# Optimization experiments

Measured on AMD Instinct MI355X. Metric: run time of the kernel, lower is better.

The kernel has to match this reference:

```python
import jax, jax.numpy as jnp
import numpy as np

B, N, DIN, A = 64, 64, 64, 32
DOUT = 128          # obs_output_dim == obs_act_output_dim == 128 (required by module wiring)
OA_IN = DIN + A     # obs_act_input_dim = 96


def _w(key, shape):
    fan_in = shape[-1]
    return jax.random.normal(key, shape, jnp.float32) / jnp.sqrt(jnp.float32(fan_in))


def setup_inputs() -> dict:
    key = jax.random.key(0)
    ks = jax.random.split(key, 14)
    return {
        "states": jax.random.normal(ks[0], (B, N, DIN), jnp.float32),
        "policies": jax.random.uniform(ks[1], (B, N, A), jnp.float32),
        "actions": jax.random.uniform(ks[2], (B, N, A), jnp.float32),
        # state_embed_preproc: Linear(obs_input_dim, 128) + LeakyReLU
        "W_se_pre": _w(ks[3], (128, DIN)),
        "b_se_pre": jnp.zeros((128,), jnp.float32),
        # key/query layers (shared between both attention stages in forward)
        "W_key": _w(ks[4], (DOUT, 128)),
        "W_query": _w(ks[5], (DOUT, 128)),
        # state_embed: Linear(obs_output_dim, 128) + LeakyReLU
        "W_se": _w(ks[6], (128, DOUT)),
        "b_se": jnp.zeros((128,), jnp.float32),
        # state_act_pol_embed: Linear(obs_act_input_dim, 128) + LeakyReLU
        "W_sap": _w(ks[7], (128, OA_IN)),
        "b_sap": jnp.zeros((128,), jnp.float32),
        # attention_value_layer: Linear(128, obs_act_output_dim)
        "W_av": _w(ks[8], (DOUT, 128)),
        # final value head
        "W_f1": _w(ks[9], (64, DOUT)),
        "W_f2": _w(ks[10], (1, 64)),
    }


def reference(states, policies, actions, W_se_pre, b_se_pre, W_key, W_query,
              W_se, b_se, W_sap, b_sap, W_av, W_f1, W_f2):
    lrelu = jax.nn.leaky_relu  # negative_slope=0.01, matches torch default
    d_k = W_key.shape[0]
    inv_sqrt_dk = 1.0 / jnp.sqrt(jnp.asarray(d_k, states.dtype))

    # stage 1: self-attention over agents on raw-state embeddings
    e = lrelu(states @ W_se_pre.T + b_se_pre)                       # [B,N,128]
    q1 = e @ W_query.T
    k1 = e @ W_key.T
    w_pre = jax.nn.softmax(jnp.einsum('bid,bjd->bij', q1, k1) * inv_sqrt_dk, axis=-1)
    # NB: attention_value_layer_preproc output is overwritten in the original forward;
    # the effective value is weight_preproc @ states_embed_preproc.
    av_pre = jnp.einsum('bij,bjd->bid', w_pre, e)                   # [B,N,128]

    # stage 2: self-attention weights over agents on re-embedded states
    se = lrelu(av_pre @ W_se.T + b_se)                              # [B,N,128]
    q2 = se @ W_query.T
    k2 = se @ W_key.T
    w = jax.nn.softmax(jnp.einsum('bid,bjd->bij', q2, k2) * inv_sqrt_dk, axis=-1)

    # obs_actions_policies[b,j,k] = (state_k, policy_k) if j==k else (state_k, action_k)
    obs_act = jnp.concatenate([states, actions], axis=-1)           # [B,N,OA_IN]
    obs_pol = jnp.concatenate([states, policies], axis=-1)
    n = states.shape[1]
    eye = jnp.eye(n, dtype=states.dtype)[None, :, :, None]          # [1,N,N,1]
    oap = eye * obs_pol[:, None, :, :] + (1.0 - eye) * obs_act[:, None, :, :]  # [B,N,N,OA_IN]

    emb = lrelu(oap @ W_sap.T + b_sap)                              # [B,N,N,128]
    av = emb @ W_av.T                                               # [B,N,N,DOUT]

    # fused form of repeat->weight->sum: node[b,i,j,d] = sum_k w[b,i,k] * av[b,j,k,d]
    node = jnp.einsum('bik,bjkd->bijd', w, av)                      # [B,N,N,DOUT]

    value = lrelu(node @ W_f1.T) @ W_f2.T                           # [B,N,N,1]
    return value, w_pre, w
```

## Files before the change

kernel.cpp:

```cpp
#include <hip/hip_runtime.h>

#define DEVFN __device__ __forceinline__

constexpr int BNN = 64 * 64 * 64;
constexpr float SCALE = 0.08838834764831845f;
constexpr float NSLOPE = 0.01f;

constexpr int OFF_WPRET = 0;
constexpr int OFF_WQT   = 8192;
constexpr int OFF_M     = 24576;
constexpr int OFF_WSET  = 40960;
constexpr int OFF_WSAPT = 57344;
constexpr int OFF_WAVT  = 69632;
constexpr int OFF_WF1T  = 86016;
constexpr int OFF_E     = 98304;
constexpr int OFF_Q     = 622592;
constexpr int OFF_ET    = 1146880;
constexpr int OFF_SET   = 1671168;
constexpr int OFF_HA    = 2195456;
constexpr int OFF_HD    = 2719744;


DEVFN void st128(int tid, const float* __restrict__ src, float* __restrict__ Bs, int rows) {
  const int n4 = rows * 32;
  for (int idx = tid; idx < n4; idx += 512) {
    const int r = idx >> 5, c = idx & 31;
    *reinterpret_cast<float4*>(&Bs[r * 132 + c * 4]) =
        *reinterpret_cast<const float4*>(&src[r * 128 + c * 4]);
  }
}

DEVFN void st64x(int tid, const float* __restrict__ src, float* __restrict__ Bs) {
  for (int idx = tid; idx < 1024; idx += 512) {
    const int r = idx >> 4, c = idx & 15;
    *reinterpret_cast<float4*>(&Bs[r * 68 + c * 4]) =
        *reinterpret_cast<const float4*>(&src[r * 64 + c * 4]);
  }
}

DEVFN void wrT(int tid, const float* __restrict__ S, float* __restrict__ dst, int rq) {
  const int fr = tid >> 2, a4 = tid & 3;
  float t[4];
#pragma unroll
  for (int i = 0; i < 4; ++i) t[i] = S[(a4 * 4 + i) * 132 + fr];
  float4 v; v.x = t[0]; v.y = t[1]; v.z = t[2]; v.w = t[3];
  *reinterpret_cast<float4*>(&dst[fr * 64 + rq * 16 + a4 * 4]) = v;
}


DEVFN void g1(int tid, const float* __restrict__ A, int lda,
              const float* __restrict__ Bs, int K, float (&acc)[4]) {
  const int c0 = (tid & 31) * 4, rg = tid >> 5;
#pragma unroll 8
  for (int k = 0; k < K; ++k) {
    const float4 bv = *reinterpret_cast<const float4*>(&Bs[k * 132 + c0]);
    const float a = A[rg * lda + k];
    acc[0] += a * bv.x; acc[1] += a * bv.y; acc[2] += a * bv.z; acc[3] += a * bv.w;
  }
}

DEVFN void g2A(int tid, const float* __restrict__ A0, const float* __restrict__ A1,
               int lda, const float* __restrict__ Bs, int K,
               float (&a0)[4], float (&a1)[4]) {
  const int c0 = (tid & 31) * 4, rg = tid >> 5;
#pragma unroll 4
  for (int k = 0; k < K; ++k) {
    const float4 bv = *reinterpret_cast<const float4*>(&Bs[k * 132 + c0]);
    const float x = A0[rg * lda + k];
    const float y = A1[rg * lda + k];
    a0[0] += x * bv.x; a0[1] += x * bv.y; a0[2] += x * bv.z; a0[3] += x * bv.w;
    a1[0] += y * bv.x; a1[1] += y * bv.y; a1[2] += y * bv.z; a1[3] += y * bv.w;
  }
}

DEVFN void gH(int tid, const float* __restrict__ A, int lda,
              const float* __restrict__ Bs, int K, float (&acc)[2]) {
  const int c0 = (tid & 31) * 2, rg = tid >> 5;
#pragma unroll 8
  for (int k = 0; k < K; ++k) {
    const float2 bv = *reinterpret_cast<const float2*>(&Bs[k * 68 + c0]);
    const float a = A[rg * lda + k];
    acc[0] += a * bv.x; acc[1] += a * bv.y;
  }
}

DEVFN void gH2(int tid, const float* __restrict__ A0, const float* __restrict__ A1,
               int lda, const float* __restrict__ Bs, int K,
               float (&a0)[2], float (&a1)[2]) {
  const int c0 = (tid & 31) * 2, rg = tid >> 5;
#pragma unroll 4
  for (int k = 0; k < K; ++k) {
    const float2 bv = *reinterpret_cast<const float2*>(&Bs[k * 68 + c0]);
    const float x = A0[rg * lda + k];
    const float y = A1[rg * lda + k];
    a0[0] += x * bv.x; a0[1] += x * bv.y;
    a1[0] += y * bv.x; a1[1] += y * bv.y;
  }
}

template<bool ACT, bool HASB>
DEVFN void epi(int tid, const float (&acc)[4], float* __restrict__ O, int ldo,
               const float* __restrict__ bias) {
  const int c0 = (tid & 31) * 4, rg = tid >> 5;
  float t[4];
#pragma unroll
  for (int i = 0; i < 4; ++i) {
    float x = acc[i];
    if constexpr (HASB) x += bias[c0 + i];
    if constexpr (ACT) x = (x > 0.f) ? x : NSLOPE * x;
    t[i] = x;
  }
  float4 v; v.x = t[0]; v.y = t[1]; v.z = t[2]; v.w = t[3];
  *reinterpret_cast<float4*>(&O[rg * ldo + c0]) = v;
}


DEVFN void score_half(int tid, const float* __restrict__ Qs, int hoff,
                      const float* __restrict__ Ks, float (&acc)[2]) {
  const int j = tid & 63, iw = tid >> 6;
#pragma unroll 2
  for (int kt = 0; kt < 64; kt += 8) {
    float qv[2][8];
#pragma unroll
    for (int r = 0; r < 2; ++r) {
      *reinterpret_cast<float4*>(&qv[r][0]) =
          *reinterpret_cast<const float4*>(&Qs[(iw * 2 + r) * 132 + hoff + kt]);
      *reinterpret_cast<float4*>(&qv[r][4]) =
          *reinterpret_cast<const float4*>(&Qs[(iw * 2 + r) * 132 + hoff + kt + 4]);
    }
#pragma unroll
    for (int kk = 0; kk < 8; ++kk) {
      const float kv = Ks[(kt + kk) * 68 + j];
      acc[0] += qv[0][kk] * kv;
      acc[1] += qv[1][kk] * kv;
    }
  }
}

DEVFN void softmax_write(int tid, float (&acc)[2], float* __restrict__ Wp,
                         float* __restrict__ gout) {
  const int j = tid & 63, iw = tid >> 6;
#pragma unroll
  for (int r = 0; r < 2; ++r) {
    float v = acc[r] * SCALE;
    float m = v;
#pragma unroll
    for (int off = 32; off > 0; off >>= 1) m = fmaxf(m, __shfl_xor(m, off, 64));
    const float p = __expf(v - m);
    float s = p;
#pragma unroll
    for (int off = 32; off > 0; off >>= 1) s += __shfl_xor(s, off, 64);
    const float w = p / s;
    Wp[(iw * 2 + r) * 68 + j] = w;
    gout[(iw * 2 + r) * 64 + j] = w;
  }
}


__global__ void transpose_all(const float* __restrict__ Wpre, const float* __restrict__ Wq,
                              const float* __restrict__ Wse, const float* __restrict__ Wsap,
                              const float* __restrict__ Wav, const float* __restrict__ Wf1,
                              float* __restrict__ ws) {
  const int m = blockIdx.y;
  const float* src; int Cout, K, off;
  switch (m) {
    case 0: src = Wpre; Cout = 128; K = 64;  off = OFF_WPRET; break;
    case 1: src = Wq;   Cout = 128; K = 128; off = OFF_WQT;   break;
    case 2: src = Wse;  Cout = 128; K = 128; off = OFF_WSET;  break;
    case 3: src = Wsap; Cout = 128; K = 96;  off = OFF_WSAPT; break;
    case 4: src = Wav;  Cout = 128; K = 128; off = OFF_WAVT;  break;
    default: src = Wf1; Cout = 64;  K = 128; off = OFF_WF1T;  break;
  }
  const int idx = blockIdx.x * 256 + threadIdx.x;
  if (idx < Cout * K) {
    const int c = idx / K, k = idx - c * K;
    ws[off + k * Cout + c] = src[idx];
  }
}

__global__ __launch_bounds__(512) void make_M(const float* __restrict__ Wkey,
                                              float* __restrict__ ws) {
  __shared__ float As[16 * 132];
  __shared__ float Bs[64 * 132];
  const int tid = threadIdx.x;
  const int r0 = blockIdx.x * 16;
  {
    const int r = tid >> 5, c = tid & 31;
    *reinterpret_cast<float4*>(&As[r * 132 + c * 4]) =
        *reinterpret_cast<const float4*>(&ws[OFF_WQT + (r0 + r) * 128 + c * 4]);
  }
  const int c0 = (tid & 31) * 4, rg = tid >> 5;
  float acc[4] = {};
  for (int h = 0; h < 2; ++h) {
    __syncthreads();
    st128(tid, Wkey + h * 8192, Bs, 64);
    __syncthreads();
#pragma unroll 8
    for (int k = 0; k < 64; ++k) {
      const float4 bv = *reinterpret_cast<const float4*>(&Bs[k * 132 + c0]);
      const float a = As[rg * 132 + h * 64 + k];
      acc[0] += a * bv.x; acc[1] += a * bv.y; acc[2] += a * bv.z; acc[3] += a * bv.w;
    }
  }
  float4 v; v.x = acc[0]; v.y = acc[1]; v.z = acc[2]; v.w = acc[3];
  *reinterpret_cast<float4*>(&ws[OFF_M + (r0 + rg) * 128 + c0]) = v;
}

__global__ __launch_bounds__(512) void P1(const float* __restrict__ states,
                                          const float* __restrict__ policies,
                                          const float* __restrict__ actions,
                                          const float* __restrict__ b_sap,
                                          const float* __restrict__ b_se_pre,
                                          float* __restrict__ ws) {
  __shared__ float S[16 * 68];
  __shared__ float Aa[16 * 36], Ap[16 * 36];
  __shared__ float Ea[16 * 132];
  __shared__ float Ep[16 * 132], Dd[16 * 132], Er[16 * 132];
  __shared__ float Bs[64 * 132];
  const int tid = threadIdx.x;
  const int wid = ((blockIdx.x & 7) << 5) | (blockIdx.x >> 3);
  const int b = wid >> 2, rq = wid & 3;
  const int r0g = b * 64 + rq * 16;

  for (int idx = tid; idx < 1024; idx += 512) {
    const int r = idx >> 6, c = idx & 63;
    S[r * 68 + c] = states[(r0g + r) * 64 + c];
  }
  {
    const int r = tid >> 5, c = tid & 31;
    Aa[r * 36 + c] = actions[(r0g + r) * 32 + c];
    Ap[r * 36 + c] = policies[(r0g + r) * 32 + c];
  }
  st128(tid, ws + OFF_WSAPT, Bs, 64);
  __syncthreads();
  float cm[4] = {};
  g1(tid, S, 68, Bs, 64, cm);
  __syncthreads();
  st128(tid, ws + OFF_WSAPT + 8192, Bs, 32);
  __syncthreads();
  float aa[4] = {cm[0], cm[1], cm[2], cm[3]};
  float ap[4] = {cm[0], cm[1], cm[2], cm[3]};
  g2A(tid, Aa, Ap, 36, Bs, 32, aa, ap);
  epi<true, true>(tid, aa, Ea, 132, b_sap);
  epi<true, true>(tid, ap, Ep, 132, b_sap);
  __syncthreads();
  for (int idx = tid; idx < 2048; idx += 512) {
    const int r = idx >> 7, c = idx & 127;
    Ep[r * 132 + c] -= Ea[r * 132 + c];
  }
  __syncthreads();
  st128(tid, ws + OFF_WAVT, Bs, 64);
  __syncthreads();
  float av[4] = {}, dl[4] = {};
  g2A(tid, Ea, Ep, 132, Bs, 64, av, dl);
  __syncthreads();
  st128(tid, ws + OFF_WAVT + 8192, Bs, 64);
  __syncthreads();
  g2A(tid, Ea + 64, Ep + 64, 132, Bs, 64, av, dl);
  __syncthreads();
  epi<false, false>(tid, av, Ea, 132, nullptr);
  epi<false, false>(tid, dl, Dd, 132, nullptr);
  __syncthreads();
  st64x(tid, ws + OFF_WF1T, Bs);
  __syncthreads();
  float ah[2] = {}, aha[2] = {};
  gH2(tid, Dd, Ea, 132, Bs, 64, ah, aha);
  __syncthreads();
  st64x(tid, ws + OFF_WF1T + 4096, Bs);
  __syncthreads();
  gH2(tid, Dd + 64, Ea + 64, 132, Bs, 64, ah, aha);
  {
    const int c0 = (tid & 31) * 2, rg = tid >> 5;
    float2 vh; vh.x = ah[0]; vh.y = ah[1];
    float2 va; va.x = aha[0]; va.y = aha[1];
    *reinterpret_cast<float2*>(&ws[OFF_HD + (r0g + rg) * 64 + c0]) = vh;
    *reinterpret_cast<float2*>(&ws[OFF_HA + (r0g + rg) * 64 + c0]) = va;
  }
  __syncthreads();
  st128(tid, ws + OFF_WPRET, Bs, 64);
  __syncthreads();
  {
    float ae[4] = {};
    g1(tid, S, 68, Bs, 64, ae);
    const int c0 = (tid & 31) * 4, rg = tid >> 5;
    float t[4];
#pragma unroll
    for (int i = 0; i < 4; ++i) {
      float x = ae[i] + b_se_pre[c0 + i];
      t[i] = (x > 0.f) ? x : NSLOPE * x;
    }
    float4 v; v.x = t[0]; v.y = t[1]; v.z = t[2]; v.w = t[3];
    *reinterpret_cast<float4*>(&Er[rg * 132 + c0]) = v;
    *reinterpret_cast<float4*>(&ws[OFF_E + (r0g + rg) * 128 + c0]) = v;
  }
  __syncthreads();
  wrT(tid, Er, ws + OFF_ET + b * 8192, rq);
  st128(tid, ws + OFF_M, Bs, 64);
  __syncthreads();
  float af[4] = {};
  g1(tid, Er, 132, Bs, 64, af);
  __syncthreads();
  st128(tid, ws + OFF_M + 8192, Bs, 64);
  __syncthreads();
  g1(tid, Er + 64, 132, Bs, 64, af);
  epi<false, false>(tid, af, ws + OFF_Q + r0g * 128, 128, nullptr);
}

__global__ __launch_bounds__(512) void P3(const float* __restrict__ b_se,
                                          float* __restrict__ ws,
                                          float* __restrict__ out) {
  __shared__ float Qs[16 * 132];
  __shared__ float Bs[64 * 132];
  __shared__ float Wp[16 * 68], AV[16 * 132], SEr[16 * 132];
  const int tid = threadIdx.x;
  const int wid = ((blockIdx.x & 7) << 5) | (blockIdx.x >> 3);
  const int b = wid >> 2, rq = wid & 3;
  const int r0g = b * 64 + rq * 16;

  {
    const int r = tid >> 5, c = tid & 31;
    *reinterpret_cast<float4*>(&Qs[r * 132 + c * 4]) =
        *reinterpret_cast<const float4*>(&ws[OFF_Q + (r0g + r) * 128 + c * 4]);
  }
  st64x(tid, ws + OFF_ET + b * 8192, Bs);
  __syncthreads();
  float sc[2] = {};
  score_half(tid, Qs, 0, Bs, sc);
  __syncthreads();
  st64x(tid, ws + OFF_ET + b * 8192 + 4096, Bs);
  __syncthreads();
  score_half(tid, Qs, 64, Bs, sc);
  softmax_write(tid, sc, Wp, out + BNN + b * 4096 + rq * 1024);
  __syncthreads();
  st128(tid, ws + OFF_E + b * 8192, Bs, 64);
  __syncthreads();
  {
    float a[4] = {};
    g1(tid, Wp, 68, Bs, 64, a);
    epi<false, false>(tid, a, AV, 132, nullptr);
  }
  __syncthreads();
  st128(tid, ws + OFF_WSET, Bs, 64);
  __syncthreads();
  float as[4] = {};
  g1(tid, AV, 132, Bs, 64, as);
  __syncthreads();
  st128(tid, ws + OFF_WSET + 8192, Bs, 64);
  __syncthreads();
  g1(tid, AV + 64, 132, Bs, 64, as);
  {
    const int c0 = (tid & 31) * 4, rg = tid >> 5;
    float t[4];
#pragma unroll
    for (int i = 0; i < 4; ++i) {
      float x = as[i] + b_se[c0 + i];
      t[i] = (x > 0.f) ? x : NSLOPE * x;
    }
    float4 v; v.x = t[0]; v.y = t[1]; v.z = t[2]; v.w = t[3];
    *reinterpret_cast<float4*>(&SEr[rg * 132 + c0]) = v;
  }
  __syncthreads();
  wrT(tid, SEr, ws + OFF_SET + b * 8192, rq);
  st128(tid, ws + OFF_M, Bs, 64);
  __syncthreads();
  float af[4] = {};
  g1(tid, SEr, 132, Bs, 64, af);
  __syncthreads();
  st128(tid, ws + OFF_M + 8192, Bs, 64);
  __syncthreads();
  g1(tid, SEr + 64, 132, Bs, 64, af);
  epi<false, false>(tid, af, ws + OFF_Q + r0g * 128, 128, nullptr);
}

__global__ __launch_bounds__(512) void P4(const float* __restrict__ Wf2g,
                                          float* __restrict__ ws,
                                          float* __restrict__ out) {
  __shared__ float Qs[16 * 132];
  __shared__ float Bs[64 * 132];
  __shared__ float Wp[16 * 68], Hb[16 * 66];
  __shared__ float Hd[64 * 69];
  __shared__ float Wf2s[64];
  const int tid = threadIdx.x;
  const int wid = ((blockIdx.x & 7) << 5) | (blockIdx.x >> 3);
  const int b = wid >> 2, rq = wid & 3;
  const int r0g = b * 64 + rq * 16;

  for (int idx = tid; idx < 4096; idx += 512)
    Hd[(idx >> 6) * 69 + (idx & 63)] = ws[OFF_HD + b * 4096 + idx];
  if (tid < 64) Wf2s[tid] = Wf2g[tid];
  {
    const int r = tid >> 5, c = tid & 31;
    *reinterpret_cast<float4*>(&Qs[r * 132 + c * 4]) =
        *reinterpret_cast<const float4*>(&ws[OFF_Q + (r0g + r) * 128 + c * 4]);
  }
  st64x(tid, ws + OFF_SET + b * 8192, Bs);
  __syncthreads();
  float sc[2] = {};
  score_half(tid, Qs, 0, Bs, sc);
  __syncthreads();
  st64x(tid, ws + OFF_SET + b * 8192 + 4096, Bs);
  __syncthreads();
  score_half(tid, Qs, 64, Bs, sc);
  softmax_write(tid, sc, Wp, out + 2 * BNN + b * 4096 + rq * 1024);
  __syncthreads();
  st64x(tid, ws + OFF_HA + b * 4096, Bs);
  __syncthreads();
  float ah[2] = {};
  gH(tid, Wp, 68, Bs, 64, ah);
  {
    const int c0 = (tid & 31) * 2, rg = tid >> 5;
    float2 v; v.x = ah[0]; v.y = ah[1];
    *reinterpret_cast<float2*>(&Hb[rg * 66 + c0]) = v;
  }
  __syncthreads();
  const int j = tid & 63, iw = tid >> 6;
  float wv[2], a2[2] = {0.f, 0.f};
#pragma unroll
  for (int r = 0; r < 2; ++r) wv[r] = Wp[(iw * 2 + r) * 68 + j];
  for (int f = 0; f < 64; ++f) {
    const float hdv = Hd[j * 69 + f];
    const float wf = Wf2s[f];
#pragma unroll
    for (int r = 0; r < 2; ++r) {
      float t = Hb[(iw * 2 + r) * 66 + f] + wv[r] * hdv;
      t = (t > 0.f) ? t : NSLOPE * t;
      a2[r] += t * wf;
    }
  }
#pragma unroll
  for (int r = 0; r < 2; ++r)
    out[(r0g + iw * 2 + r) * 64 + j] = a2[r];
}

extern "C" void kernel_launch(void* const* d_in, const int* in_sizes, int n_in,
                              void* d_out, int out_size, void* d_ws, size_t ws_size,
                              hipStream_t stream) {
  const float* states   = (const float*)d_in[0];
  const float* policies = (const float*)d_in[1];
  const float* actions  = (const float*)d_in[2];
  const float* W_se_pre = (const float*)d_in[3];
  const float* b_se_pre = (const float*)d_in[4];
  const float* W_key    = (const float*)d_in[5];
  const float* W_query  = (const float*)d_in[6];
  const float* W_se     = (const float*)d_in[7];
  const float* b_se     = (const float*)d_in[8];
  const float* W_sap    = (const float*)d_in[9];
  const float* b_sap    = (const float*)d_in[10];
  const float* W_av     = (const float*)d_in[11];
  const float* W_f1     = (const float*)d_in[12];
  const float* W_f2     = (const float*)d_in[13];
  float* out = (float*)d_out;
  float* ws  = (float*)d_ws;

  transpose_all<<<dim3(64, 6), dim3(256), 0, stream>>>(
      W_se_pre, W_query, W_se, W_sap, W_av, W_f1, ws);
  make_M<<<dim3(8), dim3(512), 0, stream>>>(W_key, ws);
  P1<<<dim3(256), dim3(512), 0, stream>>>(states, policies, actions, b_sap, b_se_pre, ws);
  P3<<<dim3(256), dim3(512), 0, stream>>>(b_se, ws, out);
  P4<<<dim3(256), dim3(512), 0, stream>>>(W_f2, ws, out);
}
```

Baseline: 64.59 us.

## Merge weight prep kernels, vectorize GEMM inner loops, enlarge shared B tiles

Fuses the weight-transpose kernel and the M=Wq^T*Wkey kernel into a single WPREP launch, with M reading Wq directly in transposed form. This removes one kernel launch and a dependency between launches. The small GEMM helpers now read the A operand as float4 and process four k-steps per iteration to cut LDS instruction count. The shared B buffer grows to 8704 floats so full 128-row K/Wf1 tiles load at once, dropping a sync-and-reload round in the score and head GEMMs at the cost of more LDS per block, which may reduce occupancy.

Result: faster. 62.17 us, median of 2 (-3.7%).

```diff
diff --git a/kernel.cpp b/kernel.cpp
--- a/kernel.cpp
+++ b/kernel.cpp
@@ -7,7 +7,6 @@
 constexpr float NSLOPE = 0.01f;
 
 constexpr int OFF_WPRET = 0;
-constexpr int OFF_WQT   = 8192;
 constexpr int OFF_M     = 24576;
 constexpr int OFF_WSET  = 40960;
 constexpr int OFF_WSAPT = 57344;
@@ -21,17 +20,28 @@
 constexpr int OFF_HD    = 2719744;
 
 
+DEVFN void fma4(float (&acc)[4], float a, const float4& bv) {
+  acc[0] += a * bv.x; acc[1] += a * bv.y; acc[2] += a * bv.z; acc[3] += a * bv.w;
+}
+DEVFN void fma2(float (&acc)[2], float a, const float2& bv) {
+  acc[0] += a * bv.x; acc[1] += a * bv.y;
+}
+
+
+template<int NT>
 DEVFN void st128(int tid, const float* __restrict__ src, float* __restrict__ Bs, int rows) {
   const int n4 = rows * 32;
-  for (int idx = tid; idx < n4; idx += 512) {
+  for (int idx = tid; idx < n4; idx += NT) {
     const int r = idx >> 5, c = idx & 31;
     *reinterpret_cast<float4*>(&Bs[r * 132 + c * 4]) =
         *reinterpret_cast<const float4*>(&src[r * 128 + c * 4]);
   }
 }
 
-DEVFN void st64x(int tid, const float* __restrict__ src, float* __restrict__ Bs) {
-  for (int idx = tid; idx < 1024; idx += 512) {
+template<int NT>
+DEVFN void st64r(int tid, const float* __restrict__ src, float* __restrict__ Bs, int rows) {
+  const int n4 = rows * 16;
+  for (int idx = tid; idx < n4; idx += NT) {
     const int r = idx >> 4, c = idx & 15;
     *reinterpret_cast<float4*>(&Bs[r * 68 + c * 4]) =
         *reinterpret_cast<const float4*>(&src[r * 64 + c * 4]);
@@ -51,11 +61,15 @@
 DEVFN void g1(int tid, const float* __restrict__ A, int lda,
               const float* __restrict__ Bs, int K, float (&acc)[4]) {
   const int c0 = (tid & 31) * 4, rg = tid >> 5;
-#pragma unroll 8
-  for (int k = 0; k < K; ++k) {
-    const float4 bv = *reinterpret_cast<const float4*>(&Bs[k * 132 + c0]);
-    const float a = A[rg * lda + k];
-    acc[0] += a * bv.x; acc[1] += a * bv.y; acc[2] += a * bv.z; acc[3] += a * bv.w;
+  const float* __restrict__ Ar = A + rg * lda;
+#pragma unroll 4
+  for (int k4 = 0; k4 < K; k4 += 4) {
+    const float4 a4 = *reinterpret_cast<const float4*>(&Ar[k4]);
+    const float4 b0 = *reinterpret_cast<const float4*>(&Bs[(k4 + 0) * 132 + c0]);
+    const float4 b1 = *reinterpret_cast<const float4*>(&Bs[(k4 + 1) * 132 + c0]);
+    const float4 b2 = *reinterpret_cast<const float4*>(&Bs[(k4 + 2) * 132 + c0]);
+    const float4 b3 = *reinterpret_cast<const float4*>(&Bs[(k4 + 3) * 132 + c0]);
+    fma4(acc, a4.x, b0); fma4(acc, a4.y, b1); fma4(acc, a4.z, b2); fma4(acc, a4.w, b3);
   }
 }
 
@@ -63,24 +77,35 @@
                int lda, const float* __restrict__ Bs, int K,
                float (&a0)[4], float (&a1)[4]) {
   const int c0 = (tid & 31) * 4, rg = tid >> 5;
-#pragma unroll 4
-  for (int k = 0; k < K; ++k) {
-    const float4 bv = *reinterpret_cast<const float4*>(&Bs[k * 132 + c0]);
-    const float x = A0[rg * lda + k];
-    const float y = A1[rg * lda + k];
-    a0[0] += x * bv.x; a0[1] += x * bv.y; a0[2] += x * bv.z; a0[3] += x * bv.w;
-    a1[0] += y * bv.x; a1[1] += y * bv.y; a1[2] += y * bv.z; a1[3] += y * bv.w;
+  const float* __restrict__ X = A0 + rg * lda;
+  const float* __restrict__ Y = A1 + rg * lda;
+#pragma unroll 2
+  for (int k4 = 0; k4 < K; k4 += 4) {
+    const float4 x4 = *reinterpret_cast<const float4*>(&X[k4]);
+    const float4 y4 = *reinterpret_cast<const float4*>(&Y[k4]);
+    const float4 b0 = *reinterpret_cast<const float4*>(&Bs[(k4 + 0) * 132 + c0]);
+    const float4 b1 = *reinterpret_cast<const float4*>(&Bs[(k4 + 1) * 132 + c0]);
+    const float4 b2 = *reinterpret_cast<const float4*>(&Bs[(k4 + 2) * 132 + c0]);
+    const float4 b3 = *reinterpret_cast<const float4*>(&Bs[(k4 + 3) * 132 + c0]);
+    fma4(a0, x4.x, b0); fma4(a1, y4.x, b0);
+    fma4(a0, x4.y, b1); fma4(a1, y4.y, b1);
+    fma4(a0, x4.z, b2); fma4(a1, y4.z, b2);
+    fma4(a0, x4.w, b3); fma4(a1, y4.w, b3);
   }
 }
 
 DEVFN void gH(int tid, const float* __restrict__ A, int lda,
               const float* __restrict__ Bs, int K, float (&acc)[2]) {
   const int c0 = (tid & 31) * 2, rg = tid >> 5;
-#pragma unroll 8
-  for (int k = 0; k < K; ++k) {
-    const float2 bv = *reinterpret_cast<const float2*>(&Bs[k * 68 + c0]);
-    const float a = A[rg * lda + k];
-    acc[0] += a * bv.x; acc[1] += a * bv.y;
+  const float* __restrict__ Ar = A + rg * lda;
+#pragma unroll 4
+  for (int k4 = 0; k4 < K; k4 += 4) {
+    const float4 a4 = *reinterpret_cast<const float4*>(&Ar[k4]);
+    const float2 b0 = *reinterpret_cast<const float2*>(&Bs[(k4 + 0) * 68 + c0]);
+    const float2 b1 = *reinterpret_cast<const float2*>(&Bs[(k4 + 1) * 68 + c0]);
+    const float2 b2 = *reinterpret_cast<const float2*>(&Bs[(k4 + 2) * 68 + c0]);
+    const float2 b3 = *reinterpret_cast<const float2*>(&Bs[(k4 + 3) * 68 + c0]);
+    fma2(acc, a4.x, b0); fma2(acc, a4.y, b1); fma2(acc, a4.z, b2); fma2(acc, a4.w, b3);
   }
 }
 
@@ -88,13 +113,20 @@
                int lda, const float* __restrict__ Bs, int K,
                float (&a0)[2], float (&a1)[2]) {
   const int c0 = (tid & 31) * 2, rg = tid >> 5;
-#pragma unroll 4
-  for (int k = 0; k < K; ++k) {
-    const float2 bv = *reinterpret_cast<const float2*>(&Bs[k * 68 + c0]);
-    const float x = A0[rg * lda + k];
-    const float y = A1[rg * lda + k];
-    a0[0] += x * bv.x; a0[1] += x * bv.y;
-    a1[0] += y * bv.x; a1[1] += y * bv.y;
+  const float* __restrict__ X = A0 + rg * lda;
+  const float* __restrict__ Y = A1 + rg * lda;
+#pragma unroll 2
+  for (int k4 = 0; k4 < K; k4 += 4) {
+    const float4 x4 = *reinterpret_cast<const float4*>(&X[k4]);
+    const float4 y4 = *reinterpret_cast<const float4*>(&Y[k4]);
+    const float2 b0 = *reinterpret_cast<const float2*>(&Bs[(k4 + 0) * 68 + c0]);
+    const float2 b1 = *reinterpret_cast<const float2*>(&Bs[(k4 + 1) * 68 + c0]);
+    const float2 b2 = *reinterpret_cast<const float2*>(&Bs[(k4 + 2) * 68 + c0]);
+    const float2 b3 = *reinterpret_cast<const float2*>(&Bs[(k4 + 3) * 68 + c0]);
+    fma2(a0, x4.x, b0); fma2(a1, y4.x, b0);
+    fma2(a0, x4.y, b1); fma2(a1, y4.y, b1);
+    fma2(a0, x4.z, b2); fma2(a1, y4.z, b2);
+    fma2(a0, x4.w, b3); fma2(a1, y4.w, b3);
   }
 }
 
@@ -115,18 +147,18 @@
 }
 
 
-DEVFN void score_half(int tid, const float* __restrict__ Qs, int hoff,
+DEVFN void score_full(int tid, const float* __restrict__ Qs,
                       const float* __restrict__ Ks, float (&acc)[2]) {
   const int j = tid & 63, iw = tid >> 6;
 #pragma unroll 2
-  for (int kt = 0; kt < 64; kt += 8) {
+  for (int kt = 0; kt < 128; kt += 8) {
     float qv[2][8];
 #pragma unroll
     for (int r = 0; r < 2; ++r) {
       *reinterpret_cast<float4*>(&qv[r][0]) =
-          *reinterpret_cast<const float4*>(&Qs[(iw * 2 + r) * 132 + hoff + kt]);
+          *reinterpret_cast<const float4*>(&Qs[(iw * 2 + r) * 132 + kt]);
       *reinterpret_cast<float4*>(&qv[r][4]) =
-          *reinterpret_cast<const float4*>(&Qs[(iw * 2 + r) * 132 + hoff + kt + 4]);
+          *reinterpret_cast<const float4*>(&Qs[(iw * 2 + r) * 132 + kt + 4]);
     }
 #pragma unroll
     for (int kk = 0; kk < 8; ++kk) {
@@ -157,53 +189,56 @@
 }
 
 
-__global__ void transpose_all(const float* __restrict__ Wpre, const float* __restrict__ Wq,
-                              const float* __restrict__ Wse, const float* __restrict__ Wsap,
-                              const float* __restrict__ Wav, const float* __restrict__ Wf1,
-                              float* __restrict__ ws) {
-  const int m = blockIdx.y;
-  const float* src; int Cout, K, off;
-  switch (m) {
-    case 0: src = Wpre; Cout = 128; K = 64;  off = OFF_WPRET; break;
-    case 1: src = Wq;   Cout = 128; K = 128; off = OFF_WQT;   break;
-    case 2: src = Wse;  Cout = 128; K = 128; off = OFF_WSET;  break;
-    case 3: src = Wsap; Cout = 128; K = 96;  off = OFF_WSAPT; break;
-    case 4: src = Wav;  Cout = 128; K = 128; off = OFF_WAVT;  break;
-    default: src = Wf1; Cout = 64;  K = 128; off = OFF_WF1T;  break;
-  }
-  const int idx = blockIdx.x * 256 + threadIdx.x;
-  if (idx < Cout * K) {
-    const int c = idx / K, k = idx - c * K;
-    ws[off + k * Cout + c] = src[idx];
-  }
-}
-
-__global__ __launch_bounds__(512) void make_M(const float* __restrict__ Wkey,
-                                              float* __restrict__ ws) {
+__global__ __launch_bounds__(512) void WPREP(const float* __restrict__ Wpre,
+                                             const float* __restrict__ Wq,
+                                             const float* __restrict__ Wkey,
+                                             const float* __restrict__ Wse,
+                                             const float* __restrict__ Wsap,
+                                             const float* __restrict__ Wav,
+                                             const float* __restrict__ Wf1,
+                                             float* __restrict__ ws) {
   __shared__ float As[16 * 132];
   __shared__ float Bs[64 * 132];
-  const int tid = threadIdx.x;
-  const int r0 = blockIdx.x * 16;
-  {
-    const int r = tid >> 5, c = tid & 31;
-    *reinterpret_cast<float4*>(&As[r * 132 + c * 4]) =
-        *reinterpret_cast<const float4*>(&ws[OFF_WQT + (r0 + r) * 128 + c * 4]);
-  }
-  const int c0 = (tid & 31) * 4, rg = tid >> 5;
-  float acc[4] = {};
-  for (int h = 0; h < 2; ++h) {
-    __syncthreads();
-    st128(tid, Wkey + h * 8192, Bs, 64);
-    __syncthreads();
+  const int tid = threadIdx.x, bid = blockIdx.x;
+  if (bid < 120) {
+    const int gt = bid * 512 + tid;
+    if (gt < 8192) {
+      const int c = gt >> 6, k = gt & 63;
+      ws[OFF_WPRET + k * 128 + c] = Wpre[gt];
+    } else if (gt < 24576) {
+      const int i = gt - 8192, c = i >> 7, k = i & 127;
+      ws[OFF_WSET + k * 128 + c] = Wse[i];
+    } else if (gt < 36864) {
+      const int i = gt - 24576, c = i / 96, k = i - c * 96;
+      ws[OFF_WSAPT + k * 128 + c] = Wsap[i];
+    } else if (gt < 53248) {
+      const int i = gt - 36864, c = i >> 7, k = i & 127;
+      ws[OFF_WAVT + k * 128 + c] = Wav[i];
+    } else if (gt < 61440) {
+      const int i = gt - 53248, c = i >> 7, k = i & 127;
+      ws[OFF_WF1T + k * 64 + c] = Wf1[i];
+    }
+  } else {
+    const int r0 = (bid - 120) * 16;
+    for (int idx = tid; idx < 2048; idx += 512) {
+      const int r = idx & 15, o = idx >> 4;
+      As[r * 132 + o] = Wq[o * 128 + r0 + r];
+    }
+    const int c0 = (tid & 31) * 4, rg = tid >> 5;
+    float acc[4] = {};
+    for (int h = 0; h < 2; ++h) {
+      __syncthreads();
+      st128<512>(tid, Wkey + h * 8192, Bs, 64);
+      __syncthreads();
 #pragma unroll 8
-    for (int k = 0; k < 64; ++k) {
-      const float4 bv = *reinterpret_cast<const float4*>(&Bs[k * 132 + c0]);
-      const float a = As[rg * 132 + h * 64 + k];
-      acc[0] += a * bv.x; acc[1] += a * bv.y; acc[2] += a * bv.z; acc[3] += a * bv.w;
-    }
-  }
-  float4 v; v.x = acc[0]; v.y = acc[1]; v.z = acc[2]; v.w = acc[3];
-  *reinterpret_cast<float4*>(&ws[OFF_M + (r0 + rg) * 128 + c0]) = v;
+      for (int k = 0; k < 64; ++k) {
+        const float4 bv = *reinterpret_cast<const float4*>(&Bs[k * 132 + c0]);
+        fma4(acc, As[rg * 132 + h * 64 + k], bv);
+      }
+    }
+    float4 v; v.x = acc[0]; v.y = acc[1]; v.z = acc[2]; v.w = acc[3];
+    *reinterpret_cast<float4*>(&ws[OFF_M + (r0 + rg) * 128 + c0]) = v;
+  }
 }
 
 __global__ __launch_bounds__(512) void P1(const float* __restrict__ states,
@@ -216,7 +251,7 @@
   __shared__ float Aa[16 * 36], Ap[16 * 36];
   __shared__ float Ea[16 * 132];
   __shared__ float Ep[16 * 132], Dd[16 * 132], Er[16 * 132];
-  __shared__ float Bs[64 * 132];
+  __shared__ float Bs[8704];
   const int tid = threadIdx.x;
   const int wid = ((blockIdx.x & 7) << 5) | (blockIdx.x >> 3);
   const int b = wid >> 2, rq = wid & 3;
@@ -231,12 +266,12 @@
     Aa[r * 36 + c] = actions[(r0g + r) * 32 + c];
     Ap[r * 36 + c] = policies[(r0g + r) * 32 + c];
   }
-  st128(tid, ws + OFF_WSAPT, Bs, 64);
+  st128<512>(tid, ws + OFF_WSAPT, Bs, 64);
   __syncthreads();
   float cm[4] = {};
   g1(tid, S, 68, Bs, 64, cm);
   __syncthreads();
-  st128(tid, ws + OFF_WSAPT + 8192, Bs, 32);
+  st128<512>(tid, ws + OFF_WSAPT + 8192, Bs, 32);
   __syncthreads();
   float aa[4] = {cm[0], cm[1], cm[2], cm[3]};
   float ap[4] = {cm[0], cm[1], cm[2], cm[3]};
@@ -249,26 +284,23 @@
     Ep[r * 132 + c] -= Ea[r * 132 + c];
   }
   __syncthreads();
-  st128(tid, ws + OFF_WAVT, Bs, 64);
+  st128<512>(tid, ws + OFF_WAVT, Bs, 64);
   __syncthreads();
   float av[4] = {}, dl[4] = {};
   g2A(tid, Ea, Ep, 132, Bs, 64, av, dl);
   __syncthreads();
-  st128(tid, ws + OFF_WAVT + 8192, Bs, 64);
+  st128<512>(tid, ws + OFF_WAVT + 8192, Bs, 64);
   __syncthreads();
   g2A(tid, Ea + 64, Ep + 64, 132, Bs, 64, av, dl);
   __syncthreads();
   epi<false, false>(tid, av, Ea, 132, nullptr);
   epi<false, false>(tid, dl, Dd, 132, nullptr);
   __syncthreads();
-  st64x(tid, ws + OFF_WF1T, Bs);
+  st64r<512>(tid, ws + OFF_WF1T, Bs, 128);
   __syncthreads();
   float ah[2] = {}, aha[2] = {};
   gH2(tid, Dd, Ea, 132, Bs, 64, ah, aha);
-  __syncthreads();
-  st64x(tid, ws + OFF_WF1T + 4096, Bs);
-  __syncthreads();
-  gH2(tid, Dd + 64, Ea + 64, 132, Bs, 64, ah, aha);
+  gH2(tid, Dd + 64, Ea + 64, 132, Bs + 64 * 68, 64, ah, aha);
   {
     const int c0 = (tid & 31) * 2, rg = tid >> 5;
     float2 vh; vh.x = ah[0]; vh.y = ah[1];
@@ -277,7 +309,7 @@
     *reinterpret_cast<float2*>(&ws[OFF_HA + (r0g + rg) * 64 + c0]) = va;
   }
   __syncthreads();
-  st128(tid, ws + OFF_WPRET, Bs, 64);
+  st128<512>(tid, ws + OFF_WPRET, Bs, 64);
   __syncthreads();
   {
     float ae[4] = {};
@@ -295,12 +327,12 @@
   }
   __syncthreads();
   wrT(tid, Er, ws + OFF_ET + b * 8192, rq);
-  st128(tid, ws + OFF_M, Bs, 64);
+  st128<512>(tid, ws + OFF_M, Bs, 64);
   __syncthreads();
   float af[4] = {};
   g1(tid, Er, 132, Bs, 64, af);
   __syncthreads();
-  st128(tid, ws + OFF_M + 8192, Bs, 64);
+  st128<512>(tid, ws + OFF_M + 8192, Bs, 64);
   __syncthreads();
   g1(tid, Er + 64, 132, Bs, 64, af);
   epi<false, false>(tid, af, ws + OFF_Q + r0g * 128, 128, nullptr);
@@ -310,7 +342,7 @@
                                           float* __restrict__ ws,
                                           float* __restrict__ out) {
   __shared__ float Qs[16 * 132];
-  __shared__ float Bs[64 * 132];
+  __shared__ float Bs[8704];
   __shared__ float Wp[16 * 68], AV[16 * 132], SEr[16 * 132];
   const int tid = threadIdx.x;
   const int wid = ((blockIdx.x & 7) << 5) | (blockIdx.x >> 3);
@@ -322,17 +354,13 @@
     *reinterpret_cast<float4*>(&Qs[r * 132 + c * 4]) =
         *reinterpret_cast<const float4*>(&ws[OFF_Q + (r0g + r) * 128 + c * 4]);
   }
-  st64x(tid, ws + OFF_ET + b * 8192, Bs);
+  st64r<512>(tid, ws + OFF_ET + b * 8192, Bs, 128);
   __syncthreads();
   float sc[2] = {};
-  score_half(tid, Qs, 0, Bs, sc);
-  __syncthreads();
-  st64x(tid, ws + OFF_ET + b * 8192 + 4096, Bs);
-  __syncthreads();
-  score_half(tid, Qs, 64, Bs, sc);
+  score_full(tid, Qs, Bs, sc);
   softmax_write(tid, sc, Wp, out + BNN + b * 4096 + rq * 1024);
   __syncthreads();
-  st128(tid, ws + OFF_E + b * 8192, Bs, 64);
+  st128<512>(tid, ws + OFF_E + b * 8192, Bs, 64);
   __syncthreads();
   {
     float a[4] = {};
@@ -340,12 +368,12 @@
     epi<false, false>(tid, a, AV, 132, nullptr);
   }
   __syncthreads();
-  st128(tid, ws + OFF_WSET, Bs, 64);
+  st128<512>(tid, ws + OFF_WSET, Bs, 64);
   __syncthreads();
   float as[4] = {};
   g1(tid, AV, 132, Bs, 64, as);
   __syncthreads();
-  st128(tid, ws + OFF_WSET + 8192, Bs, 64);
+  st128<512>(tid, ws + OFF_WSET + 8192, Bs, 64);
   __syncthreads();
   g1(tid, AV + 64, 132, Bs, 64, as);
   {
@@ -361,12 +389,12 @@
   }
   __syncthreads();
   wrT(tid, SEr, ws + OFF_SET + b * 8192, rq);
-  st128(tid, ws + OFF_M, Bs, 64);
+  st128<512>(tid, ws + OFF_M, Bs, 64);
   __syncthreads();
   float af[4] = {};
   g1(tid, SEr, 132, Bs, 64, af);
   __syncthreads();
-  st128(tid, ws + OFF_M + 8192, Bs, 64);
+  st128<512>(tid, ws + OFF_M + 8192, Bs, 64);
   __syncthreads();
   g1(tid, SEr + 64, 132, Bs, 64, af);
   epi<false, false>(tid, af, ws + OFF_Q + r0g * 128, 128, nullptr);
@@ -376,7 +404,7 @@
                                           float* __restrict__ ws,
                                           float* __restrict__ out) {
   __shared__ float Qs[16 * 132];
-  __shared__ float Bs[64 * 132];
+  __shared__ float Bs[8704];
   __shared__ float Wp[16 * 68], Hb[16 * 66];
   __shared__ float Hd[64 * 69];
   __shared__ float Wf2s[64];
@@ -393,17 +421,13 @@
     *reinterpret_cast<float4*>(&Qs[r * 132 + c * 4]) =
         *reinterpret_cast<const float4*>(&ws[OFF_Q + (r0g + r) * 128 + c * 4]);
   }
-  st64x(tid, ws + OFF_SET + b * 8192, Bs);
+  st64r<512>(tid, ws + OFF_SET + b * 8192, Bs, 128);
   __syncthreads();
   float sc[2] = {};
-  score_half(tid, Qs, 0, Bs, sc);
-  __syncthreads();
-  st64x(tid, ws + OFF_SET + b * 8192 + 4096, Bs);
-  __syncthreads();
-  score_half(tid, Qs, 64, Bs, sc);
+  score_full(tid, Qs, Bs, sc);
   softmax_write(tid, sc, Wp, out + 2 * BNN + b * 4096 + rq * 1024);
   __syncthreads();
-  st64x(tid, ws + OFF_HA + b * 4096, Bs);
+  st64r<512>(tid, ws + OFF_HA + b * 4096, Bs, 64);
   __syncthreads();
   float ah[2] = {};
   gH(tid, Wp, 68, Bs, 64, ah);
@@ -452,9 +476,8 @@
   float* out = (float*)d_out;
   float* ws  = (float*)d_ws;
 
-  transpose_all<<<dim3(64, 6), dim3(256), 0, stream>>>(
-      W_se_pre, W_query, W_se, W_sap, W_av, W_f1, ws);
-  make_M<<<dim3(8), dim3(512), 0, stream>>>(W_key, ws);
+  WPREP<<<dim3(128), dim3(512), 0, stream>>>(
+      W_se_pre, W_query, W_key, W_se, W_sap, W_av, W_f1, ws);
   P1<<<dim3(256), dim3(512), 0, stream>>>(states, policies, actions, b_sap, b_se_pre, ws);
   P3<<<dim3(256), dim3(512), 0, stream>>>(b_se, ws, out);
   P4<<<dim3(256), dim3(512), 0, stream>>>(W_f2, ws, out);
```
